# Performance work log

Hardware: AMD Instinct MI355X
Metric: run time of the kernel (lower is better)

## Reference

```python
import jax, jax.numpy as jnp
import numpy as np
import math

NUM_HEADS = 16
HIDDEN = 1024
HEAD_DIM = HIDDEN // NUM_HEADS
MAX_POS = 512
BUCKET = 256
SCALE = 1.0 / math.sqrt(3.0 * HEAD_DIM)


def _make_log_bucket_position(rel_pos):
    # rel_pos: int32 [S, S]
    mid = BUCKET // 2
    rp = rel_pos.astype(jnp.float32)
    sign = jnp.sign(rp)
    abs_pos = jnp.where((rel_pos < mid) & (rel_pos > -mid), float(mid - 1), jnp.abs(rp))
    log_pos = jnp.ceil(jnp.log(abs_pos / mid) * (mid - 1) / math.log((MAX_POS - 1) / mid)) + mid
    bucket_pos = jnp.where(abs_pos <= mid, rp, log_pos * sign)
    return bucket_pos.astype(jnp.int32)


def _get_rel_pos(num_positions):
    ids = jnp.arange(num_positions, dtype=jnp.int32)
    rel_pos = ids[:, None] - ids[None, :]  # [S, S]
    return _make_log_bucket_position(rel_pos)


def setup_inputs() -> dict:
    key = jax.random.key(0)
    ks = jax.random.split(key, 10)
    B, S = 8, 512
    s_in = 1.0 / math.sqrt(HIDDEN)
    inputs = jax.random.normal(ks[0], (B, S, HIDDEN), dtype=jnp.float32)
    rel_embeddings = jax.random.normal(ks[1], (B, 2 * BUCKET, HIDDEN), dtype=jnp.float32)
    Wq = jax.random.normal(ks[2], (HIDDEN, NUM_HEADS, HEAD_DIM), dtype=jnp.float32) * s_in
    Wk = jax.random.normal(ks[3], (HIDDEN, NUM_HEADS, HEAD_DIM), dtype=jnp.float32) * s_in
    Wv = jax.random.normal(ks[4], (HIDDEN, NUM_HEADS, HEAD_DIM), dtype=jnp.float32) * s_in
    bq = jnp.zeros((NUM_HEADS, HEAD_DIM), dtype=jnp.float32)
    bk = jnp.zeros((NUM_HEADS, HEAD_DIM), dtype=jnp.float32)
    bv = jnp.zeros((NUM_HEADS, HEAD_DIM), dtype=jnp.float32)
    Wo = jax.random.normal(ks[5], (HIDDEN, HIDDEN), dtype=jnp.float32) * s_in
    bo = jnp.zeros((HIDDEN,), dtype=jnp.float32)
    return {"inputs": inputs, "rel_embeddings": rel_embeddings,
            "Wq": Wq, "bq": bq, "Wk": Wk, "bk": bk, "Wv": Wv, "bv": bv,
            "Wo": Wo, "bo": bo}


def reference(inputs, rel_embeddings, Wq, bq, Wk, bk, Wv, bv, Wo, bo):
    B, S, _ = inputs.shape
    # projections: [B,S,H,D]
    query = jnp.einsum('bsc,chd->bshd', inputs, Wq) + bq
    key = jnp.einsum('bsc,chd->bshd', inputs, Wk) + bk
    value = jnp.einsum('bsc,chd->bshd', inputs, Wv) + bv

    # content-content scores: [B,H,S_q,S_k]
    scores = jnp.einsum('bkhd,bqhd->bhqk', key, query) * SCALE

    # relative position projections on rel_embeddings [B,P,hidden], P=2*BUCKET
    pos_query = jnp.einsum('bpc,chd->bphd', rel_embeddings, Wq) + bq
    pos_key = jnp.einsum('bpc,chd->bphd', rel_embeddings, Wk) + bk

    rel_pos = _get_rel_pos(S)  # [S,S] int32
    span = BUCKET

    # c2p: query vs pos_key -> [B,H,S,P], gather along last axis
    c2p = jnp.einsum('bphd,bqhd->bhqp', pos_key, query)
    c2p_pos = jnp.clip(rel_pos + span, 0, 2 * span - 1)  # [S,S]
    c2p_idx = jnp.broadcast_to(c2p_pos[None, None], (B, NUM_HEADS, S, S))
    c2p = jnp.take_along_axis(c2p, c2p_idx, axis=3) * SCALE

    # p2c: key vs pos_query -> [B,H,S,P], gather then transpose
    p2c = jnp.einsum('bphd,bkhd->bhkp', pos_query, key)
    p2c_pos = jnp.clip(-rel_pos + span, 0, 2 * span - 1)
    p2c_idx = jnp.broadcast_to(p2c_pos[None, None], (B, NUM_HEADS, S, S))
    p2c = jnp.take_along_axis(p2c, p2c_idx, axis=3)
    p2c = jnp.swapaxes(p2c, 2, 3) * SCALE

    scores = scores + c2p + p2c
    probs = jax.nn.softmax(scores.astype(jnp.float32), axis=-1).astype(inputs.dtype)

    # attend: [B,S,H,D] -> [B,S,hidden]
    attn_out = jnp.einsum('bhqk,bkhd->bqhd', probs, value)
    attn_out = attn_out.reshape(B, S, HIDDEN)
    return jnp.einsum('bsc,cd->bsd', attn_out, Wo) + bo
```

## Files before the change

kernel.cpp:

```cpp
#include <hip/hip_runtime.h>

#define NUM_HEADS 16
#define HEAD_DIM  64
#define HIDDEN    1024
#define SEQ       512
#define BATCH     8
#define NBH       128
#define POSN      512
#define SCALE_F   0.07216878364870323f

typedef __attribute__((ext_vector_type(8))) short  short8;
typedef __attribute__((ext_vector_type(4))) short  short4_t;
typedef __attribute__((ext_vector_type(4))) float  floatx4;

#define GLDS16(gsrc, ldst) \
    __builtin_amdgcn_global_load_lds((const __attribute__((address_space(1))) void*)(gsrc), \
                                     (__attribute__((address_space(3))) void*)(ldst), 16, 0, 0)

__device__ __forceinline__ float bits2f(short s) {
    union { unsigned u; float f; } x;
    x.u = ((unsigned)(unsigned short)s) << 16;
    return x.f;
}
__device__ __forceinline__ short f2bits(float f) {
    union { float f; unsigned u; } x;
    x.f = f;
    unsigned r = x.u + 0x7fffu + ((x.u >> 16) & 1u);
    return (short)(r >> 16);
}

__global__ __launch_bounds__(256)
void prep_all(const float* __restrict__ a, const float* __restrict__ b,
              short* __restrict__ oa, short* __restrict__ ob,
              const float* __restrict__ w0, const float* __restrict__ w1,
              const float* __restrict__ w2, const float* __restrict__ w3,
              short* __restrict__ o0, short* __restrict__ o1,
              short* __restrict__ o2, short* __restrict__ o3,
              int* __restrict__ ftab)
{
    __shared__ float tile[64][65];
    const int bid = blockIdx.x, t = threadIdx.x;

    if (bid < 4096) {
        const int idx = bid * 256 + t;
        floatx4 va = ((const floatx4*)a)[idx];
        floatx4 vb = ((const floatx4*)b)[idx];
        short4_t ra, rb;
#pragma unroll
        for (int i = 0; i < 4; i++) { ra[i] = f2bits(va[i]); rb[i] = f2bits(vb[i]); }
        ((short4_t*)oa)[idx] = ra;
        ((short4_t*)ob)[idx] = rb;
        return;
    }
    if (bid < 5120) {
        const int r = bid - 4096;
        const int z = r >> 8, rem = r & 255;
        const float* src = (z == 0) ? w0 : (z == 1) ? w1 : (z == 2) ? w2 : w3;
        short*       dst = (z == 0) ? o0 : (z == 1) ? o1 : (z == 2) ? o2 : o3;
        const int c0 = (rem & 15) * 64, n0 = (rem >> 4) * 64;
#pragma unroll
        for (int j = 0; j < 16; j++) {
            const int e = t + j * 256;
            tile[e >> 6][e & 63] = src[(long)(c0 + (e >> 6)) * 1024 + n0 + (e & 63)];
        }
        __syncthreads();
#pragma unroll
        for (int j = 0; j < 16; j++) {
            const int e = t + j * 256;
            dst[(long)(n0 + (e >> 6)) * 1024 + c0 + (e & 63)] = f2bits(tile[e & 63][e >> 6]);
        }
        return;
    }
    const int i = (bid - 5120) * 256 + t;
    if (i >= 1023) return;
    const int delta = i - 511;
    const float Cf = (float)log(511.0 / 128.0);
    float absp = (delta < 128 && delta > -128) ? 127.0f : fabsf((float)delta);
    float bucket;
    if (absp <= 128.0f) {
        bucket = (float)delta;
    } else {
        float lp = ceilf((logf(absp * (1.0f / 128.0f)) * 127.0f) / Cf) + 128.0f;
        bucket = (delta > 0) ? lp : -lp;
    }
    int bi = (int)bucket + 256;
    bi = min(max(bi, 0), 511);
    ftab[i] = bi;
}

template<int MODE>
__global__ __launch_bounds__(256)
void gemm_nt(const short* __restrict__ A, long aBatch, int lda,
             const short* __restrict__ BT, long bBatch, int ldb,
             void* __restrict__ O0, void* __restrict__ O1, void* __restrict__ O2,
             long oBatch, int ldo,
             const float* __restrict__ b0, const float* __restrict__ b1,
             const float* __restrict__ b2, int Kd,
             const short* __restrict__ A2,
             void* __restrict__ O3, void* __restrict__ O4)
{
    __shared__ __align__(16) short As[2][128 * 64];
    __shared__ __align__(16) short Bs[2][128 * 64];

    int m0, n0, yy = 0;
    bool z1 = false;
    const int z = blockIdx.z;
    if (MODE == 6) {
        const int lin = blockIdx.x + (blockIdx.y << 5);
        const int swz = (lin & 7) * 160 + (lin >> 3);
        m0 = (swz & 31) * 128;
        yy = swz >> 5;
        z1 = (yy >= 24);
        n0 = (z1 ? (yy - 24) : yy) * 128;
    } else {
        m0 = blockIdx.x * 128;
        n0 = blockIdx.y * 128;
    }

    const short* Ab;
    const short* Bb;
    if (MODE == 6) {
        Ab = z1 ? A2 : A;
        Bb = BT;
    } else {
        Ab = A + (long)z * aBatch;
        Bb = BT + (long)z * bBatch;
    }

    const int t = threadIdx.x;
    const int l = t & 63, w = t >> 6;
    const int wm = w >> 1, wn = w & 1;
    const int lr = l & 15, lg = l >> 4;

    floatx4 acc[4][4];
#pragma unroll
    for (int i = 0; i < 4; i++)
#pragma unroll
        for (int j = 0; j < 4; j++) acc[i][j] = (floatx4){0.f, 0.f, 0.f, 0.f};

#pragma unroll
    for (int j = 0; j < 4; j++) {
        const int c = (w * 4 + j) * 64 + l;
        const int row = c >> 3, pc = c & 7;
        const int cc = pc ^ (row & 7);
        GLDS16(Ab + (long)(m0 + row) * lda + cc * 8, As[0] + c * 8);
        GLDS16(Bb + (long)(n0 + row) * ldb + cc * 8, Bs[0] + c * 8);
    }
    __syncthreads();

    int cur = 0;
    for (int k0 = 0; k0 < Kd; k0 += 64, cur ^= 1) {
        if (k0 + 64 < Kd) {
            const int kn = k0 + 64;
#pragma unroll
            for (int j = 0; j < 4; j++) {
                const int c = (w * 4 + j) * 64 + l;
                const int row = c >> 3, pc = c & 7;
                const int cc = pc ^ (row & 7);
                GLDS16(Ab + (long)(m0 + row) * lda + kn + cc * 8, As[cur ^ 1] + c * 8);
                GLDS16(Bb + (long)(n0 + row) * ldb + kn + cc * 8, Bs[cur ^ 1] + c * 8);
            }
        }
#pragma unroll
        for (int ks = 0; ks < 2; ks++) {
            short8 af[4], bfr[4];
#pragma unroll
            for (int i = 0; i < 4; i++) {
                const int mr = wm * 64 + i * 16 + lr;
                af[i] = *(const short8*)((char*)As[cur] + mr * 128 + (((ks * 4 + lg) ^ (mr & 7)) * 16));
                const int nr = wn * 64 + i * 16 + lr;
                bfr[i] = *(const short8*)((char*)Bs[cur] + nr * 128 + (((ks * 4 + lg) ^ (nr & 7)) * 16));
            }
#pragma unroll
            for (int i = 0; i < 4; i++)
#pragma unroll
                for (int j = 0; j < 4; j++)
                    acc[i][j] = __builtin_amdgcn_mfma_f32_16x16x32_bf16(af[i], bfr[j], acc[i][j], 0, 0, 0);
        }
        __syncthreads();
    }

    if (MODE == 6 && !z1 && yy >= 16) {
        short* tp = &As[0][0];
#pragma unroll
        for (int i = 0; i < 4; i++)
#pragma unroll
            for (int j = 0; j < 4; j++)
#pragma unroll
                for (int e = 0; e < 4; e++) {
                    const int ml  = wm * 64 + i * 16 + lg * 4 + e;
                    const int ngl = wn * 64 + j * 16 + lr;
                    const float v = acc[i][j][e] + b2[(n0 & 1023) + ngl];
                    tp[ngl * 128 + (ml ^ ((ngl & 7) << 4))] = f2bits(v);
                }
        __syncthreads();
        const int b = m0 >> 9, s0 = m0 & 511;
        const int hb = (n0 & 1023) >> 6;
        short* dst = (short*)O2;
#pragma unroll
        for (int j = 0; j < 8; j++) {
            const int task = t + j * 256;
            const int r = task >> 4, c = task & 15;
            short8 v8 = *(const short8*)(tp + r * 128 + ((c * 8) ^ ((r & 7) << 4)));
            const int h = hb + (r >> 6), d = r & 63;
            *(short8*)(dst + ((long)((b * NUM_HEADS + h) * HEAD_DIM + d)) * SEQ + s0 + c * 8) = v8;
        }
        return;
    }

#pragma unroll
    for (int i = 0; i < 4; i++) {
#pragma unroll
        for (int j = 0; j < 4; j++) {
#pragma unroll
            for (int e = 0; e < 4; e++) {
                const int mg = m0 + wm * 64 + i * 16 + lg * 4 + e;
                const int ng = n0 + wn * 64 + j * 16 + lr;
                float v = acc[i][j][e];
                if (MODE == 1) {
                    ((short*)O0)[(long)z * oBatch + (long)mg * ldo + ng] = f2bits(v);
                } else if (MODE == 2) {
                    ((float*)O0)[(long)mg * ldo + ng] = v + b0[ng];
                } else if (MODE == 6) {
                    const int hh = ng & 1023, mat = ng >> 10;
                    const int h = hh >> 6, d = hh & 63;
                    const int b = mg >> 9, s = mg & 511;
                    v += (mat == 0 ? b0 : b1)[hh];
                    short* dst;
                    if (z1) dst = (short*)(mat == 0 ? O3 : O4);
                    else    dst = (short*)(mat == 0 ? O0 : O1);
                    dst[((long)(b * NUM_HEADS + h) * SEQ + s) * HEAD_DIM + d] = f2bits(v);
                }
            }
        }
    }
}

__global__ __launch_bounds__(512, 2)
void p2c_fused(const short* __restrict__ posQ, const short* __restrict__ K,
               const short* __restrict__ c2pf, const int* __restrict__ ftab,
               short* __restrict__ Bias)
{
    __shared__ __align__(16) short As[512 * 64];
    __shared__ __align__(16) short Bs[64 * 64];
    __shared__ short ft[1024];
    const int ko = blockIdx.x, bh = blockIdx.y;
    const int k0 = ko * 64;
    const int t = threadIdx.x, l = t & 63, w = t >> 6;
    const int lr = l & 15, lg = l >> 4;
    const short* Ab = posQ + (long)bh * SEQ * HEAD_DIM;
    const short* Kb = K + (long)bh * SEQ * HEAD_DIM;
    const short* c2pb = c2pf + (long)bh * SEQ * POSN;

    for (int i = t; i < 1024; i += 512) ft[i] = (short)((i < 1023) ? ftab[i] : 0);

#pragma unroll
    for (int j = 0; j < 8; j++) {
        const int c = j * 512 + t;
        const int row = c >> 3, pc = c & 7;
        const int cc = pc ^ (row & 7);
        GLDS16(Ab + (long)row * HEAD_DIM + cc * 8, As + c * 8);
    }
    {
        const int c = t;
        const int row = c >> 3, pc = c & 7;
        const int cc = pc ^ (row & 7);
        GLDS16(Kb + (long)(k0 + row) * HEAD_DIM + cc * 8, Bs + c * 8);
    }
    __syncthreads();

    floatx4 acc[4][4];
#pragma unroll
    for (int i = 0; i < 4; i++)
#pragma unroll
        for (int j = 0; j < 4; j++) acc[i][j] = (floatx4){0.f, 0.f, 0.f, 0.f};
#pragma unroll
    for (int ks = 0; ks < 2; ks++) {
        short8 af[4], bfr[4];
#pragma unroll
        for (int i = 0; i < 4; i++) {
            const int mr = w * 64 + i * 16 + lr;
            af[i] = *(const short8*)((char*)As + mr * 128 + (((ks * 4 + lg) ^ (mr & 7)) * 16));
            const int nr = i * 16 + lr;
            bfr[i] = *(const short8*)((char*)Bs + nr * 128 + (((ks * 4 + lg) ^ (nr & 7)) * 16));
        }
#pragma unroll
        for (int i = 0; i < 4; i++)
#pragma unroll
            for (int j = 0; j < 4; j++)
                acc[i][j] = __builtin_amdgcn_mfma_f32_16x16x32_bf16(af[i], bfr[j], acc[i][j], 0, 0, 0);
    }
    __syncthreads();

#pragma unroll
    for (int i = 0; i < 4; i++)
#pragma unroll
        for (int j = 0; j < 4; j++)
#pragma unroll
            for (int e = 0; e < 4; e++) {
                const int p = w * 64 + i * 16 + lg * 4 + e;
                const int kk = j * 16 + lr;
                As[p * 64 + (kk ^ (lg << 4))] = f2bits(acc[i][j][e]);
            }
    __syncthreads();

    short* Bb = Bias + (long)bh * SEQ * SEQ;
#pragma unroll
    for (int j = 0; j < 8; j++) {
        const int task = j * 512 + t;
        const int qt = task >> 8;
        const int kl = (task >> 2) & 63;
        const int rc = task & 3;
        const int k  = k0 + kl;
        short8 v;
#pragma unroll
        for (int i = 0; i < 8; i++) {
            const int q  = qt * 32 + rc * 8 + i;
            const int fk = (int)ft[q - k + 511];
            const float sv = bits2f(As[fk * 64 + (kl ^ (((fk >> 2) & 3) << 4))]);
            const float cv = bits2f(c2pb[(long)q * POSN + fk]);
            v[i] = f2bits(sv + cv);
        }
        *(short8*)(Bb + (((long)qt * 512 + k) << 5) + rc * 8) = v;
    }
}

__global__ __launch_bounds__(256, 4)
void attn_fused(const short* __restrict__ Q, const short* __restrict__ K,
                const short* __restrict__ Vt, const short* __restrict__ Bias,
                short* __restrict__ attnO)
{
    __shared__ __align__(16) short PS[32 * 512];
    __shared__ float red[4][32];

    const int lin  = blockIdx.x;
    const int lin2 = (lin & 7) * 256 + (lin >> 3);
    const int bh = lin2 >> 4, qt = lin2 & 15;
    const int q0 = qt * 32;
    const int t = threadIdx.x, l = t & 63, w = t >> 6;
    const int lr = l & 15, lg = l >> 4;
    const long pbase = (long)bh * SEQ * HEAD_DIM;
    const short* Qb  = Q  + pbase;
    const short* Kb  = K  + pbase;
    const short* Vtb = Vt + pbase;
    const short* Bb  = Bias + ((long)bh * 16 + qt) * (512 * 32);

    short4_t bfrag[2][8];
#pragma unroll
    for (int mt = 0; mt < 2; mt++)
#pragma unroll
        for (int nt = 0; nt < 8; nt++) {
            const int k = w * 128 + nt * 16 + lr;
            bfrag[mt][nt] = *(const short4_t*)(Bb + (long)k * 32 + mt * 16 + lg * 4);
        }

    short8 aq[2][2];
#pragma unroll
    for (int mt = 0; mt < 2; mt++)
#pragma unroll
        for (int ks = 0; ks < 2; ks++)
            aq[mt][ks] = *(const short8*)(Qb + (q0 + mt * 16 + lr) * 64 + ks * 32 + lg * 8);

    floatx4 acc[2][8];
#pragma unroll
    for (int mt = 0; mt < 2; mt++)
#pragma unroll
        for (int nt = 0; nt < 8; nt++) acc[mt][nt] = (floatx4){0.f, 0.f, 0.f, 0.f};

#pragma unroll
    for (int nt = 0; nt < 8; nt++) {
        const int kr = w * 128 + nt * 16 + lr;
        short8 kb0 = *(const short8*)(Kb + kr * 64 + lg * 8);
        short8 kb1 = *(const short8*)(Kb + kr * 64 + 32 + lg * 8);
#pragma unroll
        for (int mt = 0; mt < 2; mt++) {
            acc[mt][nt] = __builtin_amdgcn_mfma_f32_16x16x32_bf16(aq[mt][0], kb0, acc[mt][nt], 0, 0, 0);
            acc[mt][nt] = __builtin_amdgcn_mfma_f32_16x16x32_bf16(aq[mt][1], kb1, acc[mt][nt], 0, 0, 0);
        }
    }

#pragma unroll
    for (int mt = 0; mt < 2; mt++)
#pragma unroll
        for (int e = 0; e < 4; e++) {
            const int r = mt * 16 + lg * 4 + e;
            float s = 0.f;
#pragma unroll
            for (int nt = 0; nt < 8; nt++) {
                float p = __expf((acc[mt][nt][e] + bits2f(bfrag[mt][nt][e])) * SCALE_F);
                acc[mt][nt][e] = p;
                s += p;
            }
            s += __shfl_xor(s, 1); s += __shfl_xor(s, 2);
            s += __shfl_xor(s, 4); s += __shfl_xor(s, 8);
            red[w][r] = s;
#pragma unroll
            for (int nt = 0; nt < 8; nt++) {
                const int kcol = w * 128 + nt * 16 + lr;
                int byte = r * 1024 + kcol * 2;
                byte ^= (r & 7) << 4;
                *(short*)((char*)PS + byte) = f2bits(acc[mt][nt][e]);
            }
        }
    __syncthreads();

    floatx4 accO[2];
    accO[0] = (floatx4){0.f, 0.f, 0.f, 0.f};
    accO[1] = (floatx4){0.f, 0.f, 0.f, 0.f};
#pragma unroll
    for (int ks = 0; ks < 16; ks++) {
        short8 vb = *(const short8*)(Vtb + (long)(w * 16 + lr) * SEQ + ks * 32 + lg * 8);
#pragma unroll
        for (int mt = 0; mt < 2; mt++) {
            const int qr = mt * 16 + lr;
            int byte = qr * 1024 + (ks * 32 + lg * 8) * 2;
            byte ^= (qr & 7) << 4;
            short8 pa = *(const short8*)((char*)PS + byte);
            accO[mt] = __builtin_amdgcn_mfma_f32_16x16x32_bf16(pa, vb, accO[mt], 0, 0, 0);
        }
    }

    const int b = bh >> 4, h = bh & 15;
#pragma unroll
    for (int mt = 0; mt < 2; mt++)
#pragma unroll
        for (int e = 0; e < 4; e++) {
            const int r = mt * 16 + lg * 4 + e;
            const float rs = red[0][r] + red[1][r] + red[2][r] + red[3][r];
            const float v = accO[mt][e] / rs;
            attnO[((long)(b * SEQ + q0 + r)) * HIDDEN + h * HEAD_DIM + w * 16 + lr] = f2bits(v);
        }
}

extern "C" void kernel_launch(void* const* d_in, const int* in_sizes, int n_in,
                              void* d_out, int out_size, void* d_ws, size_t ws_size,
                              hipStream_t stream)
{
    const float* inputs = (const float*)d_in[0];
    const float* rel    = (const float*)d_in[1];
    const float* Wq     = (const float*)d_in[2];
    const float* bq     = (const float*)d_in[3];
    const float* Wk     = (const float*)d_in[4];
    const float* bk     = (const float*)d_in[5];
    const float* Wv     = (const float*)d_in[6];
    const float* bv     = (const float*)d_in[7];
    const float* Wo     = (const float*)d_in[8];
    const float* bo     = (const float*)d_in[9];
    float* out = (float*)d_out;

    char* ws = (char*)d_ws;
    size_t off = 0;
    auto alloc = [&](size_t bytes) -> char* {
        char* p = ws + off;
        off += (bytes + 255) & ~(size_t)255;
        return p;
    };
    short* inA   = (short*)alloc(4194304ull * 2);
    short* inRel = (short*)alloc(4194304ull * 2);
    short* WqT   = (short*)alloc(1048576ull * 2);
    short* WkT   = (short*)alloc(1048576ull * 2);
    short* WvT   = (short*)alloc(1048576ull * 2);
    short* WoT   = (short*)alloc(1048576ull * 2);
    short* Qw    = (short*)alloc(4194304ull * 2);
    short* Kw    = (short*)alloc(4194304ull * 2);
    short* Vtw   = (short*)alloc(4194304ull * 2);
    short* posQw = (short*)alloc(4194304ull * 2);
    short* posKw = (short*)alloc(4194304ull * 2);
    short* c2pW  = (short*)alloc(33554432ull * 2);
    short* BW    = (short*)alloc(33554432ull * 2);
    short* attnW = (short*)alloc(4194304ull * 2);
    int*   ftabW = (int*)alloc(4096);

    prep_all<<<5124, 256, 0, stream>>>(inputs, rel, inA, inRel,
                                       Wq, Wk, Wv, Wo, WqT, WkT, WvT, WoT, ftabW);

    gemm_nt<6><<<dim3(32, 40), 256, 0, stream>>>(inA, 0, 1024, WqT, 0, 1024,
                                                 Qw, Kw, Vtw, 0, 0, bq, bk, bv, 1024,
                                                 inRel, posQw, posKw);

    gemm_nt<1><<<dim3(4, 4, 128), 256, 0, stream>>>(Qw, 32768, 64, posKw, 32768, 64,
                                                    c2pW, nullptr, nullptr, 262144, 512,
                                                    nullptr, nullptr, nullptr, 64,
                                                    nullptr, nullptr, nullptr);

    p2c_fused<<<dim3(8, 128), 512, 0, stream>>>(posQw, Kw, c2pW, ftabW, BW);

    attn_fused<<<2048, 256, 0, stream>>>(Qw, Kw, Vtw, BW, attnW);

    gemm_nt<2><<<dim3(32, 8), 256, 0, stream>>>(attnW, 0, 1024, WoT, 0, 1024,
                                                out, nullptr, nullptr, 0, 1024, bo, nullptr, nullptr, 1024,
                                                nullptr, nullptr, nullptr);
}
```

Before: 198.5 us.

## Use triple-buffered K=32 LDS pipeline with one barrier per stage in GEMM

Replaces the double-buffered K=64 tile loop in the generic NT GEMM with a three-stage ring buffer of K=32 slices. Each stage waits on vmcnt with a single barrier and prefetches two stages ahead, so more global-to-LDS loads are in flight and there is one fewer sync per tile. LDS use drops from 64KB to 48KB, which may allow higher occupancy. The cost is more loop iterations with fewer MFMAs each, plus hand-written waitcnt/sched_barrier code that has to stay correct for every GEMM mode.

```diff
diff --git a/kernel.cpp b/kernel.cpp
--- a/kernel.cpp
+++ b/kernel.cpp
@@ -99,8 +99,7 @@
              const short* __restrict__ A2,
              void* __restrict__ O3, void* __restrict__ O4)
 {
-    __shared__ __align__(16) short As[2][128 * 64];
-    __shared__ __align__(16) short Bs[2][128 * 64];
+    __shared__ __align__(16) short LB[24576];
 
     int m0, n0, yy = 0;
     bool z1 = false;
@@ -132,56 +131,66 @@
     const int wm = w >> 1, wn = w & 1;
     const int lr = l & 15, lg = l >> 4;
 
+    const int c0c = t, c1c = t + 256;
+    const int r0 = c0c >> 2, cc0 = (c0c & 3) ^ (r0 & 3);
+    const int r1 = c1c >> 2, cc1 = (c1c & 3) ^ (r1 & 3);
+
     floatx4 acc[4][4];
 #pragma unroll
     for (int i = 0; i < 4; i++)
 #pragma unroll
         for (int j = 0; j < 4; j++) acc[i][j] = (floatx4){0.f, 0.f, 0.f, 0.f};
 
-#pragma unroll
-    for (int j = 0; j < 4; j++) {
-        const int c = (w * 4 + j) * 64 + l;
-        const int row = c >> 3, pc = c & 7;
-        const int cc = pc ^ (row & 7);
-        GLDS16(Ab + (long)(m0 + row) * lda + cc * 8, As[0] + c * 8);
-        GLDS16(Bb + (long)(n0 + row) * ldb + cc * 8, Bs[0] + c * 8);
+    const int niter = Kd >> 5;
+
+    {
+        GLDS16(Ab + (long)(m0 + r0) * lda + cc0 * 8, LB + c0c * 8);
+        GLDS16(Ab + (long)(m0 + r1) * lda + cc1 * 8, LB + c1c * 8);
+        GLDS16(Bb + (long)(n0 + r0) * ldb + cc0 * 8, LB + 12288 + c0c * 8);
+        GLDS16(Bb + (long)(n0 + r1) * ldb + cc1 * 8, LB + 12288 + c1c * 8);
+        GLDS16(Ab + (long)(m0 + r0) * lda + 32 + cc0 * 8, LB + 4096 + c0c * 8);
+        GLDS16(Ab + (long)(m0 + r1) * lda + 32 + cc1 * 8, LB + 4096 + c1c * 8);
+        GLDS16(Bb + (long)(n0 + r0) * ldb + 32 + cc0 * 8, LB + 12288 + 4096 + c0c * 8);
+        GLDS16(Bb + (long)(n0 + r1) * ldb + 32 + cc1 * 8, LB + 12288 + 4096 + c1c * 8);
+    }
+
+    int cbase = 0;
+    int ibase = 8192;
+    for (int i = 0; i < niter; i++) {
+        __builtin_amdgcn_sched_barrier(0);
+        if (i + 1 < niter) { asm volatile("s_waitcnt vmcnt(4)" ::: "memory"); }
+        else               { asm volatile("s_waitcnt vmcnt(0)" ::: "memory"); }
+        __builtin_amdgcn_s_barrier();
+        __builtin_amdgcn_sched_barrier(0);
+        if (i + 2 < niter) {
+            const int kn = (i + 2) << 5;
+            GLDS16(Ab + (long)(m0 + r0) * lda + kn + cc0 * 8, LB + ibase + c0c * 8);
+            GLDS16(Ab + (long)(m0 + r1) * lda + kn + cc1 * 8, LB + ibase + c1c * 8);
+            GLDS16(Bb + (long)(n0 + r0) * ldb + kn + cc0 * 8, LB + 12288 + ibase + c0c * 8);
+            GLDS16(Bb + (long)(n0 + r1) * ldb + kn + cc1 * 8, LB + 12288 + ibase + c1c * 8);
+        }
+        const short* Asb = LB + cbase;
+        const short* Bsb = LB + 12288 + cbase;
+        short8 af[4], bfr[4];
+#pragma unroll
+        for (int i4 = 0; i4 < 4; i4++) {
+            const int mr = wm * 64 + i4 * 16 + lr;
+            af[i4] = *(const short8*)((const char*)Asb + mr * 64 + ((lg ^ (mr & 3)) * 16));
+            const int nr = wn * 64 + i4 * 16 + lr;
+            bfr[i4] = *(const short8*)((const char*)Bsb + nr * 64 + ((lg ^ (nr & 3)) * 16));
+        }
+#pragma unroll
+        for (int i4 = 0; i4 < 4; i4++)
+#pragma unroll
+            for (int j4 = 0; j4 < 4; j4++)
+                acc[i4][j4] = __builtin_amdgcn_mfma_f32_16x16x32_bf16(af[i4], bfr[j4], acc[i4][j4], 0, 0, 0);
+        cbase += 4096; if (cbase == 12288) cbase = 0;
+        ibase += 4096; if (ibase == 12288) ibase = 0;
     }
     __syncthreads();
 
-    int cur = 0;
-    for (int k0 = 0; k0 < Kd; k0 += 64, cur ^= 1) {
-        if (k0 + 64 < Kd) {
-            const int kn = k0 + 64;
-#pragma unroll
-            for (int j = 0; j < 4; j++) {
-                const int c = (w * 4 + j) * 64 + l;
-                const int row = c >> 3, pc = c & 7;
-                const int cc = pc ^ (row & 7);
-                GLDS16(Ab + (long)(m0 + row) * lda + kn + cc * 8, As[cur ^ 1] + c * 8);
-                GLDS16(Bb + (long)(n0 + row) * ldb + kn + cc * 8, Bs[cur ^ 1] + c * 8);
-            }
-        }
-#pragma unroll
-        for (int ks = 0; ks < 2; ks++) {
-            short8 af[4], bfr[4];
-#pragma unroll
-            for (int i = 0; i < 4; i++) {
-                const int mr = wm * 64 + i * 16 + lr;
-                af[i] = *(const short8*)((char*)As[cur] + mr * 128 + (((ks * 4 + lg) ^ (mr & 7)) * 16));
-                const int nr = wn * 64 + i * 16 + lr;
-                bfr[i] = *(const short8*)((char*)Bs[cur] + nr * 128 + (((ks * 4 + lg) ^ (nr & 7)) * 16));
-            }
-#pragma unroll
-            for (int i = 0; i < 4; i++)
-#pragma unroll
-                for (int j = 0; j < 4; j++)
-                    acc[i][j] = __builtin_amdgcn_mfma_f32_16x16x32_bf16(af[i], bfr[j], acc[i][j], 0, 0, 0);
-        }
-        __syncthreads();
-    }
-
     if (MODE == 6 && !z1 && yy >= 16) {
-        short* tp = &As[0][0];
+        short* tp = &LB[0];
 #pragma unroll
         for (int i = 0; i < 4; i++)
 #pragma unroll
```

Result: no change. 197.0 us (-0.8%).
